# Kernel optimization log

Hardware: AMD Instinct MI355X
Metric: run time of the kernel (lower is better)

Reference implementation:

```python
import jax, jax.numpy as jnp
import numpy as np

P, B, NB, NC = 256, 16, 1024, 37
L = 24  # max pairs per image == torch.mode-count for sorted im_idx (matches counts in setup_inputs)
DREL = 1936


def _linear(x, w, b):
    return x @ w.T + b


def _conv(x, w, b, stride, pad):
    y = jax.lax.conv_general_dilated(x, w, (stride, stride), [(pad, pad), (pad, pad)],
                                     dimension_numbers=('NCHW', 'OIHW', 'NCHW'))
    return y + b[None, :, None, None]


def _bn(x, g, bt, m, v):
    # eval-mode BatchNorm2d, eps=1e-5
    return g[None, :, None, None] * (x - m[None, :, None, None]) * jax.lax.rsqrt(v[None, :, None, None] + 1e-5) + bt[None, :, None, None]


def setup_inputs() -> dict:
    key = jax.random.key(0)
    ks = jax.random.split(key, 24)
    counts = np.concatenate([np.full(8, 8), np.full(8, 24)])  # sums to P=256, max = L = 24
    im_idx = jnp.asarray(np.repeat(np.arange(B), counts), dtype=jnp.int32)
    s = 0.02
    return {
        'features': jax.random.normal(ks[0], (NB, 2048), jnp.float32),
        'pair_idx': jax.random.randint(ks[1], (P, 2), 0, NB, jnp.int32),
        'im_idx': im_idx,
        'labels': jax.random.randint(ks[2], (NB,), 0, NC, jnp.int32),
        'union_feat': jax.random.normal(ks[3], (P, 1024, 7, 7), jnp.float32),
        'spatial_masks': jax.random.uniform(ks[4], (P, 2, 27, 27), jnp.float32),
        'w_union': jax.random.normal(ks[5], (256, 1024), jnp.float32) * s,
        'b_union': jnp.zeros((256,), jnp.float32),
        'conv1_w': jax.random.normal(ks[6], (128, 2, 7, 7), jnp.float32) * 0.05,
        'conv1_b': jnp.zeros((128,), jnp.float32),
        'bn1_g': jnp.ones((128,), jnp.float32),
        'bn1_b': jnp.zeros((128,), jnp.float32),
        'bn1_m': jnp.zeros((128,), jnp.float32),
        'bn1_v': jnp.ones((128,), jnp.float32),
        'conv2_w': jax.random.normal(ks[7], (256, 128, 3, 3), jnp.float32) * 0.05,
        'conv2_b': jnp.zeros((256,), jnp.float32),
        'bn2_g': jnp.ones((256,), jnp.float32),
        'bn2_b': jnp.zeros((256,), jnp.float32),
        'bn2_m': jnp.zeros((256,), jnp.float32),
        'bn2_v': jnp.ones((256,), jnp.float32),
        'subj_w': jax.random.normal(ks[8], (512, 2048), jnp.float32) * s,
        'subj_b': jnp.zeros((512,), jnp.float32),
        'obj_w': jax.random.normal(ks[9], (512, 2048), jnp.float32) * s,
        'obj_b': jnp.zeros((512,), jnp.float32),
        'vr_w': jax.random.normal(ks[10], (512, 12544), jnp.float32) * s,
        'vr_b': jnp.zeros((512,), jnp.float32),
        'emb1': jax.random.normal(ks[11], (NC, 200), jnp.float32),
        'emb2': jax.random.normal(ks[12], (NC, 200), jnp.float32),
        'bil_w': jax.random.normal(ks[13], (712, 712, 712), jnp.float32) * (1.0 / 712.0),
        'bil_b': jnp.zeros((712,), jnp.float32),
        'lin_w': jax.random.normal(ks[14], (712, 1424), jnp.float32) * s,
        'lin_b': jnp.zeros((712,), jnp.float32),
        'proj_w': jax.random.normal(ks[15], (1424, 1424), jnp.float32) * s,
        'proj_b': jnp.zeros((1424,), jnp.float32),
        'ac_w': jax.random.normal(ks[16], (157, 1936), jnp.float32) * s,
        'ac_b': jnp.zeros((157,), jnp.float32),
    }


def reference(features, pair_idx, im_idx, labels, union_feat, spatial_masks,
              w_union, b_union, conv1_w, conv1_b, bn1_g, bn1_b, bn1_m, bn1_v,
              conv2_w, conv2_b, bn2_g, bn2_b, bn2_m, bn2_v,
              subj_w, subj_b, obj_w, obj_b, vr_w, vr_b, emb1, emb2,
              bil_w, bil_b, lin_w, lin_b, proj_w, proj_b, ac_w, ac_b):
    # ragged gathers over pairs
    subj_rep = _linear(features[pair_idx[:, 0]], subj_w, subj_b)  # [P,512]
    obj_rep = _linear(features[pair_idx[:, 1]], obj_w, obj_b)    # [P,512]

    # union_func1 is a 1x1 conv -> channel contraction
    u = jnp.einsum('nchw,oc->nohw', union_feat, w_union) + b_union[None, :, None, None]
    x = jax.nn.relu(_conv(spatial_masks, conv1_w, conv1_b, 2, 3))        # [P,128,14,14]
    x = _bn(x, bn1_g, bn1_b, bn1_m, bn1_v)
    x = jax.lax.reduce_window(x, -jnp.inf, jax.lax.max, (1, 1, 3, 3), (1, 1, 2, 2),
                              ((0, 0), (0, 0), (1, 1), (1, 1)))          # [P,128,7,7]
    x = jax.nn.relu(_conv(x, conv2_w, conv2_b, 1, 1))                    # [P,256,7,7]
    x = _bn(x, bn2_g, bn2_b, bn2_m, bn2_v)
    vr = _linear((u + x).reshape(P, 256 * 49), vr_w, vr_b)               # [P,512]

    s = jnp.concatenate([subj_rep, emb1[labels[pair_idx[:, 0]]]], axis=1)  # [P,712]
    o = jnp.concatenate([obj_rep, emb2[labels[pair_idx[:, 1]]]], axis=1)   # [P,712]

    # nn.Bilinear over all pairs at once (per-row op, so the per-image loop vectorizes away)
    bil = jnp.einsum('nh,oht,nt->no', s, bil_w, o) + bil_b               # [P,712]
    z = _linear(jnp.concatenate([s, o], axis=1), lin_w, lin_b)           # [P,712]
    z = _linear(jax.nn.relu(jnp.concatenate([z, bil], axis=1)), proj_w, proj_b)  # [P,1424]
    rel = jnp.concatenate([z, vr], axis=1)                               # [P,1936]

    counts = jax.ops.segment_sum(jnp.ones((P,), jnp.int32), im_idx, num_segments=B)
    pooled = jax.ops.segment_max(rel, im_idx, num_segments=B)            # pool_type='max'
    starts = jnp.cumsum(counts) - counts
    pos = jnp.arange(P, dtype=jnp.int32) - starts[im_idx]                # position within image group
    memory = jnp.zeros((L, B, DREL), rel.dtype).at[pos, im_idx].set(rel)
    mask = (jnp.arange(L)[None, :] >= counts[:, None]).astype(jnp.uint8)  # [B,L]

    act = jax.nn.sigmoid(_linear(pooled, ac_w, ac_b))                    # [B,157]
    return act, pooled, memory, mask
```

## Files before the change

### kernel.cpp

```cpp
#include <hip/hip_runtime.h>
#include <math.h>

#define DEV __device__ __forceinline__

#define PP    256
#define BIMG  16
#define HB    712
#define KBIL  (712*712)
#define KSTEPS (KBIL/32)
#define DRELC 1936
#define BILSPLIT 61
#define BILCH   260

#define SZ_ACT    (16*157)
#define OFF_ACT   0
#define OFF_POOLED (SZ_ACT)
#define SZ_POOLED (16*1936)
#define OFF_MEM   (OFF_POOLED + SZ_POOLED)
#define SZ_MEM    (24*16*1936)
#define OFF_MASK  (OFF_MEM + SZ_MEM)
#define SZ_MASK   (16*24)

#define OFF_S     0
#define OFF_O     (OFF_S + 256*712)
#define OFF_Z1    (OFF_O + 256*712)
#define OFF_BIL   (OFF_Z1 + 256*712)
#define OFF_REL   (OFF_BIL + 256*712)
#define OFF_UBUF  (OFF_REL + 256*1936)
#define OFF_XP    (OFF_UBUF + 12544*256)
#define OFF_SHARED (OFF_XP + 256*128*49)
#define OFF_X1    OFF_SHARED
#define OFF_PVR   OFF_SHARED
#define OFF_PBIL  OFF_UBUF
#define OFF_PLIN  OFF_UBUF
#define OFF_PPROJ OFF_UBUF
#define SZ_SHARED (256*128*196)
#define OFF_INTS  (OFF_SHARED + SZ_SHARED)

typedef __bf16 bf16x8 __attribute__((ext_vector_type(8)));
typedef float  f32x4  __attribute__((ext_vector_type(4)));

struct Araw { float s0, s1; float4 o00, o01, o10, o11; };

__global__ __launch_bounds__(256, 4) void bil_mfma_k(
    const float* __restrict__ s, const float* __restrict__ o,
    const float* __restrict__ W, float* __restrict__ part) {
  __shared__ __align__(16) __bf16 Wsh[2][64*40];

  const int tid = threadIdx.x;
  const int C0 = blockIdx.x * 64;
  const int rowBase = blockIdx.y * 128;
  const int z0 = blockIdx.z * BILCH;
  const int zEnd = min(KSTEPS, z0 + BILCH);

  const int srow = tid >> 2;
  const int koff = (tid & 3) * 8;
  const int sc = C0 + srow;
  const float* wbase = (sc < 712) ? (W + (size_t)sc * KBIL + koff) : (const float*)0;

  const int wv = tid >> 6, lane = tid & 63;
  const int lr = lane & 15, lg = lane >> 4;
  const int n0 = rowBase + wv * 32 + lr;

  f32x4 acc[2][4];
  #pragma unroll
  for (int a = 0; a < 2; a++)
    #pragma unroll
    for (int b = 0; b < 4; b++) { acc[a][b][0]=0.f; acc[a][b][1]=0.f; acc[a][b][2]=0.f; acc[a][b][3]=0.f; }

  auto wload = [&](int z, float4& va, float4& vb) {
    if (wbase) {
      const float* p = wbase + (size_t)z * 32;
      va = *(const float4*)p;
      vb = *(const float4*)(p + 4);
    } else {
      va = make_float4(0.f,0.f,0.f,0.f);
      vb = make_float4(0.f,0.f,0.f,0.f);
    }
  };
  auto wstore = [&](int buf, const float4& va, const float4& vb) {
    float t[8] = {va.x, va.y, va.z, va.w, vb.x, vb.y, vb.z, vb.w};
    bf16x8 hi;
    #pragma unroll
    for (int i = 0; i < 8; i++) hi[i] = (__bf16)t[i];
    *(bf16x8*)&Wsh[buf][srow*40 + koff] = hi;
  };
  auto aload = [&](int z, Araw& a) {
    const int kk = z * 32 + lg * 8;
    const int h = kk / 712;
    const int t = kk - h * 712;
    const float* or0 = o + n0 * 712 + t;
    const float* or1 = o + (n0 + 16) * 712 + t;
    a.s0 = s[n0 * 712 + h];
    a.s1 = s[(n0 + 16) * 712 + h];
    a.o00 = *(const float4*)or0; a.o01 = *(const float4*)(or0 + 4);
    a.o10 = *(const float4*)or1; a.o11 = *(const float4*)(or1 + 4);
  };
  auto amake = [&](const Araw& a, bf16x8 (&ahi)[2]) {
    float p0[8] = {a.o00.x,a.o00.y,a.o00.z,a.o00.w, a.o01.x,a.o01.y,a.o01.z,a.o01.w};
    float p1[8] = {a.o10.x,a.o10.y,a.o10.z,a.o10.w, a.o11.x,a.o11.y,a.o11.z,a.o11.w};
    #pragma unroll
    for (int i = 0; i < 8; i++) {
      ahi[0][i] = (__bf16)(a.s0 * p0[i]);
      ahi[1][i] = (__bf16)(a.s1 * p1[i]);
    }
  };
  auto domfma = [&](int buf, bf16x8 (&ahi)[2]) {
    #pragma unroll
    for (int cf = 0; cf < 4; cf++) {
      bf16x8 bhi = *(bf16x8*)&Wsh[buf][(cf*16 + lr)*40 + lg*8];
      #pragma unroll
      for (int rf = 0; rf < 2; rf++) {
        acc[rf][cf] = __builtin_amdgcn_mfma_f32_16x16x32_bf16(ahi[rf], bhi, acc[rf][cf], 0, 0, 0);
      }
    }
  };

  Araw A0, A1;
  {
    float4 pa, pb;
    wload(z0, pa, pb);
    aload(z0, A0);
    wstore(0, pa, pb);
  }
  float4 s0a, s0b, s1a, s1b;
  wload(min(z0 + 1, zEnd - 1), s0a, s0b);
  wload(min(z0 + 2, zEnd - 1), s1a, s1b);
  __syncthreads();

  int z = z0;
  for (; z + 1 < zEnd; z += 2) {
    aload(z + 1, A1);
    {
      bf16x8 ahi[2];
      amake(A0, ahi);
      domfma(0, ahi);
    }
    wstore(1, s0a, s0b);
    wload(min(z + 3, zEnd - 1), s0a, s0b);
    __syncthreads();
    aload(min(z + 2, zEnd - 1), A0);
    {
      bf16x8 ahi[2];
      amake(A1, ahi);
      domfma(1, ahi);
    }
    wstore(0, s1a, s1b);
    wload(min(z + 4, zEnd - 1), s1a, s1b);
    __syncthreads();
  }
  if (z < zEnd) {
    bf16x8 ahi[2];
    amake(A0, ahi);
    domfma(0, ahi);
  }

  const int bz = blockIdx.z;
  #pragma unroll
  for (int rf = 0; rf < 2; rf++) {
    #pragma unroll
    for (int cf = 0; cf < 4; cf++) {
      const int c = C0 + cf*16 + lr;
      if (c >= 712) continue;
      #pragma unroll
      for (int i = 0; i < 4; i++) {
        const int n = rowBase + wv*32 + rf*16 + lg*4 + i;
        part[((size_t)bz*256 + n)*712 + c] = acc[rf][cf][i];
      }
    }
  }
}

struct GP {
  const float* A; const float* A2; const float* B; const float* bias;
  float* C;
  const int* gidx; int goff;
  int M, N, K;
  int ldc, coff;
  int kChunk;
  const float* bn_g; const float* bn_b; const float* bn_m; const float* bn_v;
  const float* B2; const float* bias2; float* C2;
};


template<int MODE>
DEV float loadA(const GP& p, int r, int k) {
  if (MODE == 0) { int fr = p.gidx[2*r + (int)blockIdx.z]; return p.A[fr*2048 + k]; }
  if (MODE == 2 || MODE == 8) return p.A[r*p.K + k];
  if (MODE == 3) return (k < 712) ? p.A[r*712 + k] : p.A2[r*712 + (k-712)];
  if (MODE == 4) { float v = (k < 712) ? p.A[r*712 + k] : p.A2[r*712 + (k-712)];
                   return fmaxf(v, 0.f); }
  if (MODE == 5) { int n = r/49, q = r - n*49; return p.A[(n*1024 + k)*49 + q]; }
  if (MODE == 6) {
    int n = r/49, q = r - n*49; int py = q/7, px = q - py*7;
    int ic = k/9, k9 = k - ic*9; int dy = k9/3, dx = k9 - dy*3;
    int iy = py + dy - 1, ix = px + dx - 1;
    if ((unsigned)iy >= 7u || (unsigned)ix >= 7u) return 0.f;
    return p.A[(n*128 + ic)*49 + iy*7 + ix];
  }
  return 0.f;
}

template<int MODE>
DEV float loadB(const GP& p, int c, int k) {
  if (MODE == 0) { const float* Bp = blockIdx.z ? p.B2 : p.B; return Bp[c*p.K + k]; }
  return p.B[c*p.K + k];
}

template<int MODE>
__global__ __launch_bounds__(256) void gemm_k(GP p) {
  __shared__ __align__(16) __bf16 Ash[2][64*44];
  __shared__ __align__(16) __bf16 Bsh[2][64*44];
  const int tid = threadIdx.x;
  const int srow = tid & 63, koff = (tid >> 6) * 8;
  const int col0 = blockIdx.x * 64, row0 = blockIdx.y * 64;
  const int kStart = (MODE == 0) ? 0 : blockIdx.z * p.kChunk;
  const int kEnd = min(p.K, kStart + p.kChunk);
  const int wv = tid >> 6, lane = tid & 63;
  const int lr = lane & 15, lg = lane >> 4;
  const int rh = wv >> 1, ch = wv & 1;

  f32x4 acc[2][2];
  #pragma unroll
  for (int a = 0; a < 2; a++)
    #pragma unroll
    for (int b = 0; b < 2; b++) { acc[a][b][0]=0.f; acc[a][b][1]=0.f; acc[a][b][2]=0.f; acc[a][b][3]=0.f; }

  for (int kb = kStart; kb < kEnd; kb += 32) {
    {
      const int gr = row0 + srow;
      float v[8];
      #pragma unroll
      for (int i = 0; i < 8; i++) {
        const int gk = kb + koff + i;
        v[i] = (gr < p.M && gk < kEnd) ? loadA<MODE>(p, gr, gk) : 0.f;
      }
      bf16x8 hi, lo;
      #pragma unroll
      for (int i = 0; i < 8; i++) {
        __bf16 h = (__bf16)v[i];
        hi[i] = h;
        lo[i] = (__bf16)(v[i] - (float)h);
      }
      *(bf16x8*)&Ash[0][srow*44 + koff] = hi;
      *(bf16x8*)&Ash[1][srow*44 + koff] = lo;
    }
    {
      const int gc = col0 + srow;
      float v[8];
      #pragma unroll
      for (int i = 0; i < 8; i++) {
        const int gk = kb + koff + i;
        v[i] = (gc < p.N && gk < kEnd) ? loadB<MODE>(p, gc, gk) : 0.f;
      }
      bf16x8 hi, lo;
      #pragma unroll
      for (int i = 0; i < 8; i++) {
        __bf16 h = (__bf16)v[i];
        hi[i] = h;
        lo[i] = (__bf16)(v[i] - (float)h);
      }
      *(bf16x8*)&Bsh[0][srow*44 + koff] = hi;
      *(bf16x8*)&Bsh[1][srow*44 + koff] = lo;
    }
    __syncthreads();
    #pragma unroll
    for (int rf = 0; rf < 2; rf++) {
      bf16x8 ahi = *(const bf16x8*)&Ash[0][(rh*32 + rf*16 + lr)*44 + lg*8];
      bf16x8 alo = *(const bf16x8*)&Ash[1][(rh*32 + rf*16 + lr)*44 + lg*8];
      #pragma unroll
      for (int cf = 0; cf < 2; cf++) {
        bf16x8 bhi = *(const bf16x8*)&Bsh[0][(ch*32 + cf*16 + lr)*44 + lg*8];
        bf16x8 blo = *(const bf16x8*)&Bsh[1][(ch*32 + cf*16 + lr)*44 + lg*8];
        acc[rf][cf] = __builtin_amdgcn_mfma_f32_16x16x32_bf16(ahi, bhi, acc[rf][cf], 0, 0, 0);
        acc[rf][cf] = __builtin_amdgcn_mfma_f32_16x16x32_bf16(ahi, blo, acc[rf][cf], 0, 0, 0);
        acc[rf][cf] = __builtin_amdgcn_mfma_f32_16x16x32_bf16(alo, bhi, acc[rf][cf], 0, 0, 0);
      }
    }
    __syncthreads();
  }

  #pragma unroll
  for (int rf = 0; rf < 2; rf++) {
    #pragma unroll
    for (int cf = 0; cf < 2; cf++) {
      const int c = col0 + ch*32 + cf*16 + lr;
      if (c >= p.N) continue;
      #pragma unroll
      for (int i = 0; i < 4; i++) {
        const int r = row0 + rh*32 + rf*16 + lg*4 + i;
        if (r >= p.M) continue;
        float v = acc[rf][cf][i];
        if (MODE == 2 || MODE == 3 || MODE == 4) {
          p.C[(size_t)blockIdx.z * p.M * p.N + (size_t)r * p.N + c] = v;
        } else if (MODE == 5) {
          int n = r/49, q = r - n*49;
          p.C[n*12544 + c*49 + q] = v + p.bias[c];
        } else if (MODE == 6) {
          int n = r/49, q = r - n*49;
          float sc = p.bn_g[c] / sqrtf(p.bn_v[c] + 1e-5f);
          float sh = p.bn_b[c] - p.bn_m[c]*sc;
          float t2 = fmaxf(v + p.bias[c], 0.f)*sc + sh;
          p.C[n*12544 + c*49 + q] += t2;
        } else if (MODE == 8) {
          float t2 = v + p.bias[c];
          p.C[r*p.ldc + p.coff + c] = 1.f/(1.f + expf(-t2));
        } else {
          const float* bb = blockIdx.z ? p.bias2 : p.bias;
          float* Cp = blockIdx.z ? p.C2 : p.C;
          Cp[r*p.ldc + p.coff + c] = v + bb[c];
        }
      }
    }
  }
}

__global__ __launch_bounds__(256) void reduce_k(const float* __restrict__ part,
    const float* __restrict__ bias, float* __restrict__ out,
    int S, int MN, int N, int ldc, int coff) {
  int i = blockIdx.x*256 + threadIdx.x;
  if (i >= MN) return;
  float s = 0.f;
  for (int z = 0; z < S; z++) s += part[(size_t)z*MN + i];
  int r = i / N, c = i - r*N;
  out[r*ldc + coff + c] = s + bias[c];
}

__global__ __launch_bounds__(256) void emb_k(const int* __restrict__ pi,
    const int* __restrict__ labels, const float* __restrict__ e1,
    const float* __restrict__ e2, float* __restrict__ s, float* __restrict__ o) {
  int i = blockIdx.x*256 + threadIdx.x;
  if (i >= 2*256*200) return;
  int which = i / (256*200); int rest = i - which*(256*200);
  int n = rest / 200; int j = rest - n*200;
  int lab = labels[pi[2*n + which]];
  float v = which ? e2[lab*200 + j] : e1[lab*200 + j];
  (which ? o : s)[n*712 + 512 + j] = v;
}

__global__ __launch_bounds__(256) void conv1_k(const float* __restrict__ in,
    const float* __restrict__ w, const float* __restrict__ bias,
    const float* __restrict__ g, const float* __restrict__ bt,
    const float* __restrict__ m, const float* __restrict__ vv,
    float* __restrict__ out) {
  int idx = blockIdx.x*256 + threadIdx.x;
  if (idx >= 256*128*14) return;
  int oy = idx % 14; int t = idx / 14; int c = t & 127; int n = t >> 7;
  float acc[14];
  float b0 = bias[c];
  #pragma unroll
  for (int ox = 0; ox < 14; ox++) acc[ox] = b0;
  for (int ci = 0; ci < 2; ci++) {
    #pragma unroll
    for (int ky = 0; ky < 7; ky++) {
      int iy = oy*2 - 3 + ky;
      if ((unsigned)iy >= 27u) continue;
      const float* ir = in + ((n*2 + ci)*27 + iy)*27;
      const float* wr = w + ((c*2 + ci)*7 + ky)*7;
      float iv[27];
      #pragma unroll
      for (int x = 0; x < 27; x++) iv[x] = ir[x];
      float wk[7];
      #pragma unroll
      for (int kx = 0; kx < 7; kx++) wk[kx] = wr[kx];
      #pragma unroll
      for (int kx = 0; kx < 7; kx++)
        #pragma unroll
        for (int ox = 0; ox < 14; ox++) {
          int ix = ox*2 - 3 + kx;
          if (ix >= 0 && ix < 27) acc[ox] += iv[ix]*wk[kx];
        }
    }
  }
  float sc = g[c] / sqrtf(vv[c] + 1e-5f);
  float sh = bt[c] - m[c]*sc;
  float* orow = out + ((n*128 + c)*14 + oy)*14;
  #pragma unroll
  for (int ox = 0; ox < 14; ox++) orow[ox] = fmaxf(acc[ox], 0.f)*sc + sh;
}

__global__ __launch_bounds__(256) void pool_k(const float* __restrict__ x1,
                                              float* __restrict__ xp) {
  int idx = blockIdx.x*256 + threadIdx.x;
  if (idx >= 256*128*49) return;
  int px = idx % 7; int t = idx / 7; int py = t % 7; t /= 7;
  int c = t & 127; int n = t >> 7;
  float mx = -INFINITY;
  for (int dy = 0; dy < 3; dy++) {
    int y = py*2 - 1 + dy;
    if ((unsigned)y >= 14u) continue;
    for (int dx = 0; dx < 3; dx++) {
      int x = px*2 - 1 + dx;
      if ((unsigned)x >= 14u) continue;
      mx = fmaxf(mx, x1[((n*128 + c)*14 + y)*14 + x]);
    }
  }
  xp[((n*128 + c)*7 + py)*7 + px] = mx;
}

__global__ __launch_bounds__(256) void seg_k(const int* __restrict__ im,
    int* __restrict__ counts, int* __restrict__ starts, int* __restrict__ pos) {
  __shared__ int c[16], s[16];
  int tid = threadIdx.x;
  if (tid < 16) c[tid] = 0;
  __syncthreads();
  atomicAdd(&c[im[tid]], 1);
  __syncthreads();
  if (tid == 0) { int run = 0; for (int b = 0; b < 16; b++) { s[b] = run; run += c[b]; } }
  __syncthreads();
  if (tid < 16) { counts[tid] = c[tid]; starts[tid] = s[tid]; }
  pos[tid] = tid - s[im[tid]];
}

__global__ __launch_bounds__(256) void zeromask_k(float* __restrict__ out,
                                                  const int* __restrict__ counts) {
  int i = blockIdx.x*256 + threadIdx.x;
  if (i < SZ_MEM) { out[OFF_MEM + i] = 0.f; return; }
  int j = i - SZ_MEM;
  if (j < SZ_MASK) {
    int b = j / 24, l = j - b*24;
    out[OFF_MASK + j] = (l >= counts[b]) ? 1.f : 0.f;
  }
}

__global__ __launch_bounds__(256) void scatter_k(const float* __restrict__ rel,
    const int* __restrict__ pos, const int* __restrict__ im, float* __restrict__ out) {
  int n = blockIdx.x;
  int l = pos[n], b = im[n];
  float* dst = out + OFF_MEM + ((size_t)l*16 + b)*1936;
  const float* src = rel + (size_t)n*1936;
  for (int d = threadIdx.x; d < 1936; d += 256) dst[d] = src[d];
}

__global__ __launch_bounds__(256) void pooled_k(const float* __restrict__ rel,
    const int* __restrict__ starts, const int* __restrict__ counts,
    float* __restrict__ out) {
  int b = blockIdx.y;
  int d = blockIdx.x*256 + threadIdx.x;
  if (d >= 1936) return;
  int st = starts[b], ct = counts[b];
  float mx = -INFINITY;
  for (int i = 0; i < ct; i++) mx = fmaxf(mx, rel[(size_t)(st + i)*1936 + d]);
  out[OFF_POOLED + b*1936 + d] = mx;
}

extern "C" void kernel_launch(void* const* d_in, const int* in_sizes, int n_in,
                              void* d_out, int out_size, void* d_ws, size_t ws_size,
                              hipStream_t stream) {
  const float* features   = (const float*)d_in[0];
  const int*   pair_idx   = (const int*)d_in[1];
  const int*   im_idx     = (const int*)d_in[2];
  const int*   labels     = (const int*)d_in[3];
  const float* union_feat = (const float*)d_in[4];
  const float* spatial    = (const float*)d_in[5];
  const float* w_union    = (const float*)d_in[6];
  const float* b_union    = (const float*)d_in[7];
  const float* conv1_w    = (const float*)d_in[8];
  const float* conv1_b    = (const float*)d_in[9];
  const float* bn1_g      = (const float*)d_in[10];
  const float* bn1_b      = (const float*)d_in[11];
  const float* bn1_m      = (const float*)d_in[12];
  const float* bn1_v      = (const float*)d_in[13];
  const float* conv2_w    = (const float*)d_in[14];
  const float* conv2_b    = (const float*)d_in[15];
  const float* bn2_g      = (const float*)d_in[16];
  const float* bn2_b      = (const float*)d_in[17];
  const float* bn2_m      = (const float*)d_in[18];
  const float* bn2_v      = (const float*)d_in[19];
  const float* subj_w     = (const float*)d_in[20];
  const float* subj_b     = (const float*)d_in[21];
  const float* obj_w      = (const float*)d_in[22];
  const float* obj_b      = (const float*)d_in[23];
  const float* vr_w       = (const float*)d_in[24];
  const float* vr_b       = (const float*)d_in[25];
  const float* emb1       = (const float*)d_in[26];
  const float* emb2       = (const float*)d_in[27];
  const float* bil_w      = (const float*)d_in[28];
  const float* bil_b      = (const float*)d_in[29];
  const float* lin_w      = (const float*)d_in[30];
  const float* lin_b      = (const float*)d_in[31];
  const float* proj_w     = (const float*)d_in[32];
  const float* proj_b     = (const float*)d_in[33];
  const float* ac_w       = (const float*)d_in[34];
  const float* ac_b       = (const float*)d_in[35];

  float* ws = (float*)d_ws;
  float* s_mat  = ws + OFF_S;
  float* o_mat  = ws + OFF_O;
  float* z1     = ws + OFF_Z1;
  float* bilbuf = ws + OFF_BIL;
  float* rel    = ws + OFF_REL;
  float* ubuf   = ws + OFF_UBUF;
  float* x1     = ws + OFF_X1;
  float* xp     = ws + OFF_XP;
  float* pvr    = ws + OFF_PVR;
  float* pbil   = ws + OFF_PBIL;
  float* plin   = ws + OFF_PLIN;
  float* pproj  = ws + OFF_PPROJ;
  int*   ints   = (int*)(ws + OFF_INTS);
  int* counts = ints; int* starts = ints + 16; int* pos = ints + 32;
  float* out = (float*)d_out;

  dim3 blk(256);

  {
    GP g{}; g.A = features; g.gidx = pair_idx;
    g.B = subj_w;  g.bias = subj_b;  g.C = s_mat;
    g.B2 = obj_w;  g.bias2 = obj_b;  g.C2 = o_mat;
    g.M = 256; g.N = 512; g.K = 2048; g.ldc = 712; g.coff = 0; g.kChunk = 2048;
    gemm_k<0><<<dim3(8,4,2), blk, 0, stream>>>(g);
  }
  emb_k<<<dim3(400), blk, 0, stream>>>(pair_idx, labels, emb1, emb2, s_mat, o_mat);

  {
    GP g{}; g.A = union_feat; g.B = w_union; g.bias = b_union; g.C = ubuf;
    g.M = 12544; g.N = 256; g.K = 1024; g.kChunk = 1024;
    gemm_k<5><<<dim3(4,196,1), blk, 0, stream>>>(g);
  }

  conv1_k<<<dim3(1792), blk, 0, stream>>>(spatial, conv1_w, conv1_b,
                                          bn1_g, bn1_b, bn1_m, bn1_v, x1);
  pool_k<<<dim3(6272), blk, 0, stream>>>(x1, xp);

  {
    GP g{}; g.A = xp; g.B = conv2_w; g.bias = conv2_b; g.C = ubuf;
    g.M = 12544; g.N = 256; g.K = 1152; g.kChunk = 1152;
    g.bn_g = bn2_g; g.bn_b = bn2_b; g.bn_m = bn2_m; g.bn_v = bn2_v;
    gemm_k<6><<<dim3(4,196,1), blk, 0, stream>>>(g);
  }

  {
    GP g{}; g.A = ubuf; g.B = vr_w; g.C = pvr;
    g.M = 256; g.N = 512; g.K = 12544; g.kChunk = 392;
    gemm_k<2><<<dim3(8,4,32), blk, 0, stream>>>(g);
    reduce_k<<<dim3(512), blk, 0, stream>>>(pvr, vr_b, rel, 32, 256*512, 512, 1936, 1424);
  }

  {
    GP g{}; g.A = s_mat; g.A2 = o_mat; g.B = lin_w; g.C = plin;
    g.M = 256; g.N = 712; g.K = 1424; g.kChunk = 356;
    gemm_k<3><<<dim3(12,4,4), blk, 0, stream>>>(g);
    reduce_k<<<dim3(712), blk, 0, stream>>>(plin, lin_b, z1, 4, 256*712, 712, 712, 0);
  }

  bil_mfma_k<<<dim3(12, 2, BILSPLIT), dim3(256), 0, stream>>>(s_mat, o_mat, bil_w, pbil);
  reduce_k<<<dim3(712), blk, 0, stream>>>(pbil, bil_b, bilbuf, BILSPLIT, 256*712, 712, 712, 0);

  {
    GP g{}; g.A = z1; g.A2 = bilbuf; g.B = proj_w; g.C = pproj;
    g.M = 256; g.N = 1424; g.K = 1424; g.kChunk = 712;
    gemm_k<4><<<dim3(23,4,2), blk, 0, stream>>>(g);
    reduce_k<<<dim3(1424), blk, 0, stream>>>(pproj, proj_b, rel, 2, 256*1424, 1424, 1936, 0);
  }

  seg_k<<<dim3(1), blk, 0, stream>>>(im_idx, counts, starts, pos);
  zeromask_k<<<dim3((SZ_MEM + SZ_MASK + 255)/256), blk, 0, stream>>>(out, counts);
  scatter_k<<<dim3(256), blk, 0, stream>>>(rel, pos, im_idx, out);
  pooled_k<<<dim3(8,16), blk, 0, stream>>>(rel, starts, counts, out);

  {
    GP g{}; g.A = out + OFF_POOLED; g.B = ac_w; g.bias = ac_b; g.C = out + OFF_ACT;
    g.M = 16; g.N = 157; g.K = 1936; g.ldc = 157; g.coff = 0; g.kChunk = 1936;
    gemm_k<8><<<dim3(3,1,1), blk, 0, stream>>>(g);
  }
}
```

Before: 2.292 ms.

## Stream bilinear weights straight to registers and pre-convert operands to bf16

Measured after the change: 2.509 ms. +9.4%, slower.

```diff
diff --git a/kernel.cpp b/kernel.cpp
--- a/kernel.cpp
+++ b/kernel.cpp
@@ -36,135 +36,107 @@
 #define OFF_PPROJ OFF_UBUF
 #define SZ_SHARED (256*128*196)
 #define OFF_INTS  (OFF_SHARED + SZ_SHARED)
+#define OFF_OB    (OFF_INTS + 256)
+#define OFF_ST    (OFF_OB + 91136)
 
 typedef __bf16 bf16x8 __attribute__((ext_vector_type(8)));
 typedef float  f32x4  __attribute__((ext_vector_type(4)));
 
-struct Araw { float s0, s1; float4 o00, o01, o10, o11; };
-
-__global__ __launch_bounds__(256, 4) void bil_mfma_k(
-    const float* __restrict__ s, const float* __restrict__ o,
+__global__ __launch_bounds__(256) void prep_k(const float* __restrict__ s,
+    const float* __restrict__ o, __bf16* __restrict__ ob, float* __restrict__ sT) {
+  int i = blockIdx.x*256 + threadIdx.x;
+  if (i < 256*712) {
+    ob[i] = (__bf16)o[i];
+  } else {
+    int j = i - 256*712;
+    if (j < 712*256) {
+      int h = j >> 8, n = j & 255;
+      sT[j] = s[n*712 + h];
+    }
+  }
+}
+
+struct W4 { float4 a, b, c, d; };
+
+__global__ __launch_bounds__(256, 3) void bil_mfma_k(
+    const __bf16* __restrict__ ob, const float* __restrict__ sT,
     const float* __restrict__ W, float* __restrict__ part) {
-  __shared__ __align__(16) __bf16 Wsh[2][64*40];
-
   const int tid = threadIdx.x;
+  const int wv = tid >> 6, lane = tid & 63;
+  const int lr = lane & 15, lg = lane >> 4;
   const int C0 = blockIdx.x * 64;
   const int rowBase = blockIdx.y * 128;
   const int z0 = blockIdx.z * BILCH;
   const int zEnd = min(KSTEPS, z0 + BILCH);
-
-  const int srow = tid >> 2;
-  const int koff = (tid & 3) * 8;
-  const int sc = C0 + srow;
-  const float* wbase = (sc < 712) ? (W + (size_t)sc * KBIL + koff) : (const float*)0;
-
-  const int wv = tid >> 6, lane = tid & 63;
-  const int lr = lane & 15, lg = lane >> 4;
-  const int n0 = rowBase + wv * 32 + lr;
-
-  f32x4 acc[2][4];
+  const int rowHalf = wv >> 1, colHalf = wv & 1;
+  const int n0 = rowBase + rowHalf * 64;
+  const int c0 = C0 + colHalf * 32;
+  const int myc0 = c0 + lr, myc1 = c0 + 16 + lr;
+  const bool ok0 = (myc0 < 712), ok1 = (myc1 < 712);
+  const float* wp0 = W + (size_t)(ok0 ? myc0 : 711) * KBIL + lg * 8;
+  const float* wp1 = W + (size_t)(ok1 ? myc1 : 711) * KBIL + lg * 8;
+  const float4 z4 = make_float4(0.f, 0.f, 0.f, 0.f);
+
+  f32x4 acc[4][2];
   #pragma unroll
-  for (int a = 0; a < 2; a++)
-    #pragma unroll
-    for (int b = 0; b < 4; b++) { acc[a][b][0]=0.f; acc[a][b][1]=0.f; acc[a][b][2]=0.f; acc[a][b][3]=0.f; }
-
-  auto wload = [&](int z, float4& va, float4& vb) {
-    if (wbase) {
-      const float* p = wbase + (size_t)z * 32;
-      va = *(const float4*)p;
-      vb = *(const float4*)(p + 4);
-    } else {
-      va = make_float4(0.f,0.f,0.f,0.f);
-      vb = make_float4(0.f,0.f,0.f,0.f);
-    }
+  for (int rf = 0; rf < 4; rf++)
+    #pragma unroll
+    for (int cf = 0; cf < 2; cf++) { acc[rf][cf][0]=0.f; acc[rf][cf][1]=0.f; acc[rf][cf][2]=0.f; acc[rf][cf][3]=0.f; }
+
+  auto wload = [&](int z, W4& w) {
+    const float* p0 = wp0 + (size_t)z * 32;
+    const float* p1 = wp1 + (size_t)z * 32;
+    float4 a = *(const float4*)p0, b = *(const float4*)(p0 + 4);
+    float4 c = *(const float4*)p1, d = *(const float4*)(p1 + 4);
+    w.a = ok0 ? a : z4; w.b = ok0 ? b : z4;
+    w.c = ok1 ? c : z4; w.d = ok1 ? d : z4;
   };
-  auto wstore = [&](int buf, const float4& va, const float4& vb) {
-    float t[8] = {va.x, va.y, va.z, va.w, vb.x, vb.y, vb.z, vb.w};
-    bf16x8 hi;
-    #pragma unroll
-    for (int i = 0; i < 8; i++) hi[i] = (__bf16)t[i];
-    *(bf16x8*)&Wsh[buf][srow*40 + koff] = hi;
+  auto wcvt = [&](const W4& w, bf16x8& b0, bf16x8& b1) {
+    float t0[8] = {w.a.x,w.a.y,w.a.z,w.a.w, w.b.x,w.b.y,w.b.z,w.b.w};
+    float t1[8] = {w.c.x,w.c.y,w.c.z,w.c.w, w.d.x,w.d.y,w.d.z,w.d.w};
+    #pragma unroll
+    for (int i = 0; i < 8; i++) { b0[i] = (__bf16)t0[i]; b1[i] = (__bf16)t1[i]; }
   };
-  auto aload = [&](int z, Araw& a) {
+  auto astep = [&](int z, bf16x8 b0, bf16x8 b1) {
     const int kk = z * 32 + lg * 8;
     const int h = kk / 712;
     const int t = kk - h * 712;
-    const float* or0 = o + n0 * 712 + t;
-    const float* or1 = o + (n0 + 16) * 712 + t;
-    a.s0 = s[n0 * 712 + h];
-    a.s1 = s[(n0 + 16) * 712 + h];
-    a.o00 = *(const float4*)or0; a.o01 = *(const float4*)(or0 + 4);
-    a.o10 = *(const float4*)or1; a.o11 = *(const float4*)(or1 + 4);
+    #pragma unroll
+    for (int rf = 0; rf < 4; rf++) {
+      const int n = n0 + rf*16 + lr;
+      bf16x8 o8 = *(const bf16x8*)&ob[(size_t)n * 712 + t];
+      const float sv = sT[h * 256 + n];
+      bf16x8 a8;
+      #pragma unroll
+      for (int i = 0; i < 8; i++) a8[i] = (__bf16)(sv * (float)o8[i]);
+      acc[rf][0] = __builtin_amdgcn_mfma_f32_16x16x32_bf16(a8, b0, acc[rf][0], 0, 0, 0);
+      acc[rf][1] = __builtin_amdgcn_mfma_f32_16x16x32_bf16(a8, b1, acc[rf][1], 0, 0, 0);
+    }
   };
-  auto amake = [&](const Araw& a, bf16x8 (&ahi)[2]) {
-    float p0[8] = {a.o00.x,a.o00.y,a.o00.z,a.o00.w, a.o01.x,a.o01.y,a.o01.z,a.o01.w};
-    float p1[8] = {a.o10.x,a.o10.y,a.o10.z,a.o10.w, a.o11.x,a.o11.y,a.o11.z,a.o11.w};
-    #pragma unroll
-    for (int i = 0; i < 8; i++) {
-      ahi[0][i] = (__bf16)(a.s0 * p0[i]);
-      ahi[1][i] = (__bf16)(a.s1 * p1[i]);
-    }
-  };
-  auto domfma = [&](int buf, bf16x8 (&ahi)[2]) {
-    #pragma unroll
-    for (int cf = 0; cf < 4; cf++) {
-      bf16x8 bhi = *(bf16x8*)&Wsh[buf][(cf*16 + lr)*40 + lg*8];
-      #pragma unroll
-      for (int rf = 0; rf < 2; rf++) {
-        acc[rf][cf] = __builtin_amdgcn_mfma_f32_16x16x32_bf16(ahi[rf], bhi, acc[rf][cf], 0, 0, 0);
-      }
-    }
-  };
-
-  Araw A0, A1;
-  {
-    float4 pa, pb;
-    wload(z0, pa, pb);
-    aload(z0, A0);
-    wstore(0, pa, pb);
-  }
-  float4 s0a, s0b, s1a, s1b;
-  wload(min(z0 + 1, zEnd - 1), s0a, s0b);
-  wload(min(z0 + 2, zEnd - 1), s1a, s1b);
-  __syncthreads();
-
-  int z = z0;
-  for (; z + 1 < zEnd; z += 2) {
-    aload(z + 1, A1);
-    {
-      bf16x8 ahi[2];
-      amake(A0, ahi);
-      domfma(0, ahi);
-    }
-    wstore(1, s0a, s0b);
-    wload(min(z + 3, zEnd - 1), s0a, s0b);
-    __syncthreads();
-    aload(min(z + 2, zEnd - 1), A0);
-    {
-      bf16x8 ahi[2];
-      amake(A1, ahi);
-      domfma(1, ahi);
-    }
-    wstore(0, s1a, s1b);
-    wload(min(z + 4, zEnd - 1), s1a, s1b);
-    __syncthreads();
-  }
-  if (z < zEnd) {
-    bf16x8 ahi[2];
-    amake(A0, ahi);
-    domfma(0, ahi);
+
+  W4 wA, wB;
+  wload(z0, wA);
+  wload(min(z0 + 1, zEnd - 1), wB);
+  for (int z = z0; z + 1 < zEnd; z += 2) {
+    bf16x8 b0, b1;
+    wcvt(wA, b0, b1);
+    wload(min(z + 2, zEnd - 1), wA);
+    astep(z, b0, b1);
+    wcvt(wB, b0, b1);
+    wload(min(z + 3, zEnd - 1), wB);
+    astep(z + 1, b0, b1);
   }
 
   const int bz = blockIdx.z;
   #pragma unroll
-  for (int rf = 0; rf < 2; rf++) {
-    #pragma unroll
-    for (int cf = 0; cf < 4; cf++) {
-      const int c = C0 + cf*16 + lr;
-      if (c >= 712) continue;
+  for (int cf = 0; cf < 2; cf++) {
+    const int c = c0 + cf*16 + lr;
+    if (c >= 712) continue;
+    #pragma unroll
+    for (int rf = 0; rf < 4; rf++) {
       #pragma unroll
       for (int i = 0; i < 4; i++) {
-        const int n = rowBase + wv*32 + rf*16 + lg*4 + i;
+        const int n = n0 + rf*16 + lg*4 + i;
         part[((size_t)bz*256 + n)*712 + c] = acc[rf][cf][i];
       }
     }
@@ -498,6 +470,8 @@
   float* plin   = ws + OFF_PLIN;
   float* pproj  = ws + OFF_PPROJ;
   int*   ints   = (int*)(ws + OFF_INTS);
+  __bf16* obp   = (__bf16*)(ws + OFF_OB);
+  float* sTp    = ws + OFF_ST;
   int* counts = ints; int* starts = ints + 16; int* pos = ints + 32;
   float* out = (float*)d_out;
 
@@ -543,7 +517,8 @@
     reduce_k<<<dim3(712), blk, 0, stream>>>(plin, lin_b, z1, 4, 256*712, 712, 712, 0);
   }
 
-  bil_mfma_k<<<dim3(12, 2, BILSPLIT), dim3(256), 0, stream>>>(s_mat, o_mat, bil_w, pbil);
+  prep_k<<<dim3((256*712 + 712*256 + 255)/256), blk, 0, stream>>>(s_mat, o_mat, obp, sTp);
+  bil_mfma_k<<<dim3(12, 2, BILSPLIT), dim3(256), 0, stream>>>(obp, sTp, bil_w, pbil);
   reduce_k<<<dim3(712), blk, 0, stream>>>(pbil, bil_b, bilbuf, BILSPLIT, 256*712, 712, 712, 0);
 
   {
```
